# Kernel optimization log

Hardware: AMD Instinct MI355X
Metric: run time of the kernel (lower is better)

The kernel has to match this reference:

```python
import jax, jax.numpy as jnp
import numpy as np
from jax import lax

B, C, T, H, W = 1, 64, 16, 48, 48
RC = C // 16

def conv2d(x, w, b=None, stride=1, pad=1):
    out = lax.conv_general_dilated(x, w, (stride, stride), [(pad, pad), (pad, pad)],
                                   dimension_numbers=('NCHW', 'OIHW', 'NCHW'))
    return out if b is None else out + b[None, :, None, None]

def dwconv3d(x, w, b, pad, dil):
    out = lax.conv_general_dilated(x, w, (1, 1, 1), [(p, p) for p in pad], rhs_dilation=dil,
                                   dimension_numbers=('NCDHW', 'OIDHW', 'NCDHW'),
                                   feature_group_count=x.shape[1])
    return out + b[None, :, None, None, None]

def grid_sample_zeros(img, grid):
    # img [N,Cc,Hh,Ww], grid [N,Hg,Wg,2] with (x,y) in [-1,1]; bilinear, zeros padding, align_corners=False
    N, Cc, Hh, Ww = img.shape
    gx, gy = grid[..., 0], grid[..., 1]
    x = ((gx + 1.0) * Ww - 1.0) * 0.5
    y = ((gy + 1.0) * Hh - 1.0) * 0.5
    x0 = jnp.floor(x); y0 = jnp.floor(y)
    imgf = img.reshape(N, Cc, Hh * Ww)
    def corner(xi, yi, wgt):
        valid = (xi >= 0) & (xi < Ww) & (yi >= 0) & (yi < Hh)
        idx = (jnp.clip(yi, 0, Hh - 1) * Ww + jnp.clip(xi, 0, Ww - 1)).astype(jnp.int32)
        vals = jnp.take_along_axis(imgf, idx.reshape(N, 1, -1), axis=2).reshape(N, Cc, *xi.shape[1:])
        return vals * (wgt * valid)[:, None]
    return (corner(x0, y0, (x0 + 1 - x) * (y0 + 1 - y)) + corner(x0 + 1, y0, (x - x0) * (y0 + 1 - y))
            + corner(x0, y0 + 1, (x0 + 1 - x) * (y - y0)) + corner(x0 + 1, y0 + 1, (x - x0) * (y - y0)))

def corr_attn(a, w1, w2):
    avg = jnp.mean(a, axis=1, keepdims=True)
    mx = jnp.max(a, axis=1, keepdims=True)
    var = jnp.var(a, axis=1, keepdims=True, ddof=1)  # torch unbiased var
    y = jax.nn.sigmoid(conv2d(jnp.concatenate([avg, mx], axis=1), w1, pad=1) + conv2d(var, w2, pad=1))
    return a * y

def setup_inputs() -> dict:
    key = jax.random.key(0)
    ks = jax.random.split(key, 16)
    def n(k, shape, s=0.05):
        return jax.random.normal(k, shape, jnp.float32) * s
    return {
        'x': jax.random.normal(ks[0], (B, C, T, H, W), jnp.float32),
        'w_dc2': n(ks[1], (C, C)),
        'w_ofs_l': n(ks[2], (2, C, 3, 3)), 'b_ofs_l': n(ks[3], (2,)),
        'w_ofs_r': n(ks[4], (2, C, 3, 3)), 'b_ofs_r': n(ks[5], (2,)),
        'ca_w1': n(ks[6], (1, 2, 3, 3)), 'ca_w2': n(ks[7], (1, 1, 3, 3)),
        'w_down': n(ks[8], (RC, C)),
        'sa1_w': n(ks[9], (RC, 1, 9, 3, 3)), 'sa1_b': n(ks[10], (RC,)),
        'sa2_w': n(ks[11], (RC, 1, 9, 3, 3)), 'sa2_b': n(ks[12], (RC,)),
        'sa3_w': n(ks[13], (RC, 1, 9, 3, 3)), 'sa3_b': n(ks[14], (RC,)),
        'weights': jnp.ones(3, jnp.float32) / 3,
        'weights2': jnp.ones(2, jnp.float32) / 2,
        'w_back': n(ks[15], (C, RC)),
    }

def reference(x, w_dc2, w_ofs_l, b_ofs_l, w_ofs_r, b_ofs_r, ca_w1, ca_w2, w_down,
              sa1_w, sa1_b, sa2_w, sa2_b, sa3_w, sa3_b, weights, weights2, w_back):
    Bq, Cq, Tq, Hq, Wq = x.shape
    x2 = jnp.einsum('oc,bcthw->bothw', w_dc2, x)  # 1x1x1 conv3d
    left_move = jnp.concatenate([x2[:, :, 1:], x2[:, :, -1:]], axis=2)
    right_move = jnp.concatenate([x2[:, :, :1], x2[:, :, :-1]], axis=2)
    to2d = lambda t: t.transpose(0, 2, 1, 3, 4).reshape(Bq * Tq, Cq, Hq, Wq)
    off_l = conv2d(to2d(x + left_move), w_ofs_l, b_ofs_l, stride=2, pad=1)  # [BT,2,H2,W2]
    off_r = conv2d(to2d(x + right_move), w_ofs_r, b_ofs_r, stride=2, pad=1)
    H2, W2 = off_l.shape[-2:]
    gx, gy = jnp.meshgrid(jnp.arange(W2, dtype=x.dtype), jnp.arange(H2, dtype=x.dtype), indexing='xy')
    base = jnp.stack([gx, gy]) * 2.0  # [2,H2,W2]; matches create_grid_like * 2
    def norm_grid(v):  # faithful to normalize_grid (ch0 scaled by H2-1, ch1 by W2-1)
        gh = 2.0 * v[:, 0] / max(H2 - 1, 1) - 1.0
        gw = 2.0 * v[:, 1] / max(W2 - 1, 1) - 1.0
        return jnp.stack([gh, gw], axis=-1)
    left_part = grid_sample_zeros(to2d(left_move), norm_grid(base[None] + off_l))
    right_part = grid_sample_zeros(to2d(right_move), norm_grid(base[None] + off_r))
    to5d = lambda t: t.reshape(Bq, Tq, Cq, H2, W2).transpose(0, 2, 1, 3, 4)  # [B,C,T,H2,W2]
    left_part = to5d(left_part); right_part = to5d(right_part)
    def branch(part, wscale):
        aff = jnp.einsum('bcthw,bctsd->bthwsd', x, part)  # all-pairs correlation volume
        a = aff.reshape(Bq * Tq, Hq, Wq, H2 * W2).transpose(0, 3, 1, 2)
        a = corr_attn(a, ca_w1, ca_w2)
        a = a.reshape(Bq, Tq, H2, W2, Hq, Wq).transpose(0, 1, 4, 5, 2, 3)  # [B,T,H,W,H2,W2]
        return jnp.einsum('bctsd,bthwsd->bcthw', part, jax.nn.sigmoid(a) - 0.5) * wscale
    features = branch(left_part, weights2[0]) + branch(right_part, weights2[1])
    xd = jnp.einsum('oc,bcthw->bothw', w_down, x)  # channel reduction
    agg = (dwconv3d(xd, sa1_w, sa1_b, (4, 1, 1), (1, 1, 1)) * weights[0]
           + dwconv3d(xd, sa2_w, sa2_b, (4, 2, 2), (1, 2, 2)) * weights[1]
           + dwconv3d(xd, sa3_w, sa3_b, (4, 3, 3), (1, 3, 3)) * weights[2])
    agg = jnp.einsum('oc,bcthw->bothw', w_back, agg)
    return features * (jax.nn.sigmoid(agg) - 0.5)
```

## Files before the change

kernel.cpp:

```cpp
#include <hip/hip_runtime.h>
#include <hip/hip_bf16.h>

#define T_    16
#define C_    64
#define H_    48
#define W_    48
#define HW_   2304
#define THW_  36864
#define CTHW_ 2359296
#define H2_   24
#define W2_   24
#define SD_   576
#define RC_   4
#define SDT_  72

typedef short short8 __attribute__((ext_vector_type(8)));
typedef short short4v __attribute__((ext_vector_type(4)));
typedef float f32x4 __attribute__((ext_vector_type(4)));

__device__ __forceinline__ float sigm(float v) { return 1.f / (1.f + __expf(-v)); }
__device__ __forceinline__ unsigned short f2bf(float v) {
    __hip_bfloat16 h = __float2bfloat16(v);
    union { __hip_bfloat16 h; unsigned short u; } cv; cv.h = h; return cv.u;
}
__device__ __forceinline__ float bf2f(unsigned short u) {
    return __uint_as_float((unsigned)u << 16);
}

__global__ __launch_bounds__(256) void k_pre(const float* __restrict__ x,
                                             const float* __restrict__ w,
                                             const float* __restrict__ w_down,
                                             float* __restrict__ x2T,
                                             unsigned short* __restrict__ xbh,
                                             unsigned short* __restrict__ xbl,
                                             float* __restrict__ xd) {
    int base = blockIdx.x * 64;
    __shared__ float wl[64 * 65];
    __shared__ float xt[4096];
    __shared__ float ld[64 * 65];
    __shared__ float wd[256];
    int tid = threadIdx.x;
    for (int i = tid; i < 4096; i += 256) wl[(i >> 6) * 65 + (i & 63)] = w[i];
    for (int i = tid; i < 4096; i += 256) {
        float v = x[(size_t)(i >> 6) * THW_ + base + (i & 63)];
        xt[i] = v;
        ld[(i >> 6) * 65 + (i & 63)] = v;
    }
    if (tid < 256) wd[tid] = w_down[tid];
    __syncthreads();
    {
        int o_grp = tid >> 4, u_grp = tid & 15;
        float acc[4][4] = {};
        const float4* xt4 = (const float4*)xt;
        for (int c = 0; c < 64; ++c) {
            float xa[4];
            *(float4*)xa = xt4[c * 16 + u_grp];
            #pragma unroll
            for (int i = 0; i < 4; ++i) {
                float wv = wl[(o_grp * 4 + i) * 65 + c];
                #pragma unroll
                for (int g = 0; g < 4; ++g) acc[i][g] += wv * xa[g];
            }
        }
        #pragma unroll
        for (int g = 0; g < 4; ++g) {
            float4 v = make_float4(acc[0][g], acc[1][g], acc[2][g], acc[3][g]);
            *(float4*)&x2T[(size_t)(base + u_grp * 4 + g) * 64 + o_grp * 4] = v;
        }
    }
    {
        int r = tid >> 6, u = tid & 63;
        float a = 0.f;
        #pragma unroll 8
        for (int c = 0; c < 64; ++c) a += wd[r * 64 + c] * xt[c * 64 + u];
        xd[(size_t)r * THW_ + base + u] = a;
    }
    for (int i = tid; i < 4096; i += 256) {
        int u = i >> 6, c = i & 63;
        float v = ld[c * 65 + u];
        unsigned short h = f2bf(v);
        xbh[(size_t)(base + u) * 64 + c] = h;
        xbl[(size_t)(base + u) * 64 + c] = f2bf(v - bf2f(h));
    }
}

__global__ __launch_bounds__(256) void k_off(const unsigned short* __restrict__ xbh,
                                             const unsigned short* __restrict__ xbl,
                                             const float* __restrict__ x2T,
                                             const float* __restrict__ w_l,
                                             const float* __restrict__ b_l,
                                             const float* __restrict__ w_r,
                                             const float* __restrict__ b_r,
                                             float* __restrict__ off) {
    __shared__ float wlds[2304];
    int tid = threadIdx.x;
    for (int i = tid; i < 2304; i += 256) wlds[i] = (i < 1152) ? w_l[i] : w_r[i - 1152];
    __syncthreads();
    int wg = blockIdx.x * 4 + (tid >> 6);
    int lane = tid & 63;
    int j = wg % 24, i = (wg / 24) % 24, t = (wg / 576) % 16, side = wg / 9216;
    int ts = (side == 0) ? min(t + 1, T_ - 1) : max(t - 1, 0);
    const float* wp = wlds + side * 1152;
    const unsigned short* xhb = xbh + ((size_t)t * HW_) * 64 + lane;
    const unsigned short* xlb = xbl + ((size_t)t * HW_) * 64 + lane;
    const float* x2l = x2T + (size_t)ts * HW_ * 64 + lane;
    float a0 = 0.f, a1 = 0.f;
    for (int ki = 0; ki < 3; ++ki) {
        int hh = 2 * i - 1 + ki;
        if (hh < 0 || hh >= H_) continue;
        for (int kj = 0; kj < 3; ++kj) {
            int ww = 2 * j - 1 + kj;
            if (ww < 0 || ww >= W_) continue;
            int pos = hh * W_ + ww;
            float s = bf2f(xhb[(size_t)pos * 64]) + bf2f(xlb[(size_t)pos * 64])
                    + x2l[(size_t)pos * 64];
            int tap = ki * 3 + kj;
            a0 += s * wp[lane * 9 + tap];
            a1 += s * wp[576 + lane * 9 + tap];
        }
    }
    #pragma unroll
    for (int m = 32; m >= 1; m >>= 1) {
        a0 += __shfl_xor(a0, m);
        a1 += __shfl_xor(a1, m);
    }
    if (lane == 0) {
        const float* bb = (side == 0) ? b_l : b_r;
        int ob = (side * 16 + t) * 1152 + i * 24 + j;
        off[ob] = a0 + bb[0];
        off[ob + 576] = a1 + bb[1];
    }
}

__global__ __launch_bounds__(256) void k_gs(const float* __restrict__ x2T,
                                            const float* __restrict__ off,
                                            unsigned short* __restrict__ pch,
                                            unsigned short* __restrict__ pcl) {
    int wg = blockIdx.x * 4 + (threadIdx.x >> 6);
    int lane = threadIdx.x & 63;
    int sd = wg % 576;
    int t = (wg / 576) % 16;
    int side = wg / 9216;
    int d = sd % W2_, s = sd / W2_;
    const float* offp = off + (side * 16 + t) * 1152;
    float v0 = 2.f * (float)d + offp[sd];
    float v1 = 2.f * (float)s + offp[576 + sd];
    float xf = 48.f * v0 / 23.f - 0.5f;
    float yf = 48.f * v1 / 23.f - 0.5f;
    float x0 = floorf(xf), y0 = floorf(yf);
    int ix0 = (int)x0, iy0 = (int)y0;
    float fx = xf - x0, fy = yf - y0;
    float w00 = (1.f - fx) * (1.f - fy), w10 = fx * (1.f - fy);
    float w01 = (1.f - fx) * fy,         w11 = fx * fy;
    bool vx0 = (ix0 >= 0 && ix0 < W_), vx1 = (ix0 + 1 >= 0 && ix0 + 1 < W_);
    bool vy0 = (iy0 >= 0 && iy0 < H_), vy1 = (iy0 + 1 >= 0 && iy0 + 1 < H_);
    int cx0 = min(max(ix0, 0), W_ - 1), cx1 = min(max(ix0 + 1, 0), W_ - 1);
    int cy0 = min(max(iy0, 0), H_ - 1), cy1 = min(max(iy0 + 1, 0), H_ - 1);
    float m00 = (vx0 && vy0) ? w00 : 0.f;
    float m10 = (vx1 && vy0) ? w10 : 0.f;
    float m01 = (vx0 && vy1) ? w01 : 0.f;
    float m11 = (vx1 && vy1) ? w11 : 0.f;
    int ts = (side == 0) ? min(t + 1, T_ - 1) : max(t - 1, 0);
    const float* img = x2T + (size_t)ts * HW_ * 64;
    float val = m00 * img[(size_t)(cy0 * W_ + cx0) * 64 + lane]
              + m10 * img[(size_t)(cy0 * W_ + cx1) * 64 + lane]
              + m01 * img[(size_t)(cy1 * W_ + cx0) * 64 + lane]
              + m11 * img[(size_t)(cy1 * W_ + cx1) * 64 + lane];
    size_t idx = ((size_t)(side * 16 + t) * 576 + sd) * 64 + lane;
    unsigned short h = f2bf(val);
    pch[idx] = h;
    pcl[idx] = f2bf(val - bf2f(h));
}

__global__ __launch_bounds__(256) void k_stats(const unsigned short* __restrict__ xbh,
                                               const unsigned short* __restrict__ xbl,
                                               const unsigned short* __restrict__ pch,
                                               const unsigned short* __restrict__ pcl,
                                               float* __restrict__ stats) {
    int bid = blockIdx.x;
    int side = bid & 1;
    int tb = bid >> 1;
    int t = tb / 36, hwt = tb % 36;
    int base = t * HW_ + hwt * 64;
    __shared__ __attribute__((aligned(16))) unsigned short pah[2][64 * SDT_];
    __shared__ __attribute__((aligned(16))) unsigned short pal[2][64 * SDT_];
    int tid = threadIdx.x;
    int lane = tid & 63, wv = tid >> 6;
    int quad = lane >> 4, l15 = lane & 15;
    int m0 = wv * 16;
    const unsigned short* xrh = xbh + (size_t)(base + m0 + l15) * 64;
    const unsigned short* xrl = xbl + (size_t)(base + m0 + l15) * 64;
    short8 ah0 = *(const short8*)&xrh[quad * 8];
    short8 ah1 = *(const short8*)&xrh[32 + quad * 8];
    short8 al0 = *(const short8*)&xrl[quad * 8];
    short8 al1 = *(const short8*)&xrl[32 + quad * 8];
    int sH[4], sC[4];
    #pragma unroll
    for (int k = 0; k < 4; ++k) { int i = tid + k * 256; sH[k] = i >> 4; sC[k] = i & 15; }
    const unsigned short* phb = pch + (size_t)(side * 16 + t) * 576 * 64;
    const unsigned short* plb = pcl + (size_t)(side * 16 + t) * 576 * 64;
    uint2 pf_h[4], pf_l[4];
    #pragma unroll
    for (int k = 0; k < 4; ++k) {
        pf_h[k] = *(const uint2*)&phb[(size_t)sH[k] * 64 + sC[k] * 4];
        pf_l[k] = *(const uint2*)&plb[(size_t)sH[k] * 64 + sC[k] * 4];
    }
    float sum[4] = {}, sq[4] = {};
    float mx[4] = {-1e30f, -1e30f, -1e30f, -1e30f};
    for (int kt = 0; kt < 9; ++kt) {
        int b = kt & 1;
        #pragma unroll
        for (int k = 0; k < 4; ++k) {
            *(uint2*)&pah[b][sH[k] * SDT_ + sC[k] * 4] = pf_h[k];
            *(uint2*)&pal[b][sH[k] * SDT_ + sC[k] * 4] = pf_l[k];
        }
        if (kt < 8) {
            const unsigned short* ph = phb + (size_t)(kt + 1) * 64 * 64;
            const unsigned short* pl = plb + (size_t)(kt + 1) * 64 * 64;
            #pragma unroll
            for (int k = 0; k < 4; ++k) {
                pf_h[k] = *(const uint2*)&ph[(size_t)sH[k] * 64 + sC[k] * 4];
                pf_l[k] = *(const uint2*)&pl[(size_t)sH[k] * 64 + sC[k] * 4];
            }
        }
        __syncthreads();
        #pragma unroll
        for (int tile = 0; tile < 4; ++tile) {
            short8 bh0 = *(const short8*)&pah[b][(tile * 16 + l15) * SDT_ + quad * 8];
            short8 bh1 = *(const short8*)&pah[b][(tile * 16 + l15) * SDT_ + 32 + quad * 8];
            short8 bl0 = *(const short8*)&pal[b][(tile * 16 + l15) * SDT_ + quad * 8];
            short8 bl1 = *(const short8*)&pal[b][(tile * 16 + l15) * SDT_ + 32 + quad * 8];
            f32x4 dacc = {0.f, 0.f, 0.f, 0.f};
            dacc = __builtin_amdgcn_mfma_f32_16x16x32_bf16(ah0, bh0, dacc, 0, 0, 0);
            dacc = __builtin_amdgcn_mfma_f32_16x16x32_bf16(ah1, bh1, dacc, 0, 0, 0);
            dacc = __builtin_amdgcn_mfma_f32_16x16x32_bf16(ah0, bl0, dacc, 0, 0, 0);
            dacc = __builtin_amdgcn_mfma_f32_16x16x32_bf16(ah1, bl1, dacc, 0, 0, 0);
            dacc = __builtin_amdgcn_mfma_f32_16x16x32_bf16(al0, bh0, dacc, 0, 0, 0);
            dacc = __builtin_amdgcn_mfma_f32_16x16x32_bf16(al1, bh1, dacc, 0, 0, 0);
            #pragma unroll
            for (int r = 0; r < 4; ++r) {
                float v = dacc[r];
                sum[r] += v; sq[r] += v * v; mx[r] = fmaxf(mx[r], v);
            }
        }
    }
    #pragma unroll
    for (int m = 1; m < 16; m <<= 1)
        #pragma unroll
        for (int r = 0; r < 4; ++r) {
            sum[r] += __shfl_xor(sum[r], m);
            sq[r]  += __shfl_xor(sq[r], m);
            mx[r]   = fmaxf(mx[r], __shfl_xor(mx[r], m));
        }
    if (l15 == 0) {
        #pragma unroll
        for (int r = 0; r < 4; ++r) {
            int thw = base + m0 + quad * 4 + r;
            stats[(side * 3 + 0) * THW_ + thw] = sum[r] * (1.f / 576.f);
            stats[(side * 3 + 1) * THW_ + thw] = mx[r];
            stats[(side * 3 + 2) * THW_ + thw] =
                (sq[r] - sum[r] * sum[r] * (1.f / 576.f)) * (1.f / 575.f);
        }
    }
}

__global__ __launch_bounds__(256) void k_aux(const float* __restrict__ stats,
                      const float* __restrict__ ca_w1,
                      const float* __restrict__ ca_w2, float* __restrict__ yb,
                      const float* __restrict__ xd,
                      const float* __restrict__ w1, const float* __restrict__ b1,
                      const float* __restrict__ w2, const float* __restrict__ b2,
                      const float* __restrict__ w3, const float* __restrict__ b3,
                      const float* __restrict__ wts, float* __restrict__ agg0,
                      const unsigned short* __restrict__ pch,
                      unsigned short* __restrict__ partb) {
    __shared__ unsigned short ld[64 * 68];
    int blk = blockIdx.x;
    int tid = threadIdx.x;
    if (blk < (2 * THW_) / 256) {
        int idx = blk * 256 + tid;
        int side = idx / THW_, thw = idx % THW_;
        int w = thw % W_, h = (thw / W_) % H_, t = thw / HW_;
        const float* avg = stats + (side * 3 + 0) * THW_ + t * HW_;
        const float* mxp = stats + (side * 3 + 1) * THW_ + t * HW_;
        const float* var = stats + (side * 3 + 2) * THW_ + t * HW_;
        float acc = 0.f;
        for (int ki = 0; ki < 3; ++ki) {
            int hh = h - 1 + ki;
            if (hh < 0 || hh >= H_) continue;
            for (int kj = 0; kj < 3; ++kj) {
                int ww = w - 1 + kj;
                if (ww < 0 || ww >= W_) continue;
                int p = hh * W_ + ww;
                int kk = ki * 3 + kj;
                acc += ca_w1[kk] * avg[p] + ca_w1[9 + kk] * mxp[p] + ca_w2[kk] * var[p];
            }
        }
        yb[idx] = sigm(acc);
    } else if (blk < (2 * THW_) / 256 + (RC_ * THW_) / 256) {
        int idx = (blk - (2 * THW_) / 256) * 256 + tid;
        int w = idx % W_;
        int h = (idx / W_) % H_;
        int t = (idx / HW_) % T_;
        int r = idx / THW_;
        const float* xr = xd + r * THW_;
        const float* wk_arr[3] = {w1, w2, w3};
        const float* bs_arr[3] = {b1, b2, b3};
        float tot = 0.f;
        for (int m = 0; m < 3; ++m) {
            int dil = m + 1;
            float acc = bs_arr[m][r];
            const float* wk = wk_arr[m] + r * 81;
            for (int kt = 0; kt < 9; ++kt) {
                int tt = t - 4 + kt;
                if (tt < 0 || tt >= T_) continue;
                for (int kh = 0; kh < 3; ++kh) {
                    int hh = h + (kh - 1) * dil;
                    if (hh < 0 || hh >= H_) continue;
                    for (int kw = 0; kw < 3; ++kw) {
                        int wwp = w + (kw - 1) * dil;
                        if (wwp < 0 || wwp >= W_) continue;
                        acc += xr[tt * HW_ + hh * W_ + wwp] * wk[kt * 9 + kh * 3 + kw];
                    }
                }
            }
            tot += acc * wts[m];
        }
        agg0[idx] = tot;
    } else {
        int b2 = blk - ((2 * THW_) / 256 + (RC_ * THW_) / 256);
        int st = b2 / 9;
        int sdt = b2 % 9;
        const unsigned short* src = pch + ((size_t)st * 576 + sdt * 64) * 64;
        for (int i = tid; i < 4096; i += 256) ld[(i >> 6) * 68 + (i & 63)] = src[i];
        __syncthreads();
        unsigned short* dst = partb + (size_t)st * 64 * 576 + sdt * 64;
        for (int i = tid; i < 4096; i += 256) {
            int c = i >> 6, sdl = i & 63;
            dst[(size_t)c * 576 + sdl] = ld[sdl * 68 + c];
        }
    }
}

__global__ __launch_bounds__(256) void k_final(const unsigned short* __restrict__ xbh,
                                               const unsigned short* __restrict__ xbl,
                                               const unsigned short* __restrict__ pch,
                                               const unsigned short* __restrict__ pcl,
                                               const unsigned short* __restrict__ partb,
                                               const float* __restrict__ yb,
                                               const float* __restrict__ weights2,
                                               const float* __restrict__ agg0,
                                               const float* __restrict__ w_back,
                                               float* __restrict__ out) {
    int bid = blockIdx.x;
    int side = bid & 1;
    int tb = bid >> 1;
    int t = tb / 36, hwt = tb % 36;
    int base = t * HW_ + hwt * 64;
    int st = side * 16 + t;
    __shared__ __attribute__((aligned(16))) unsigned short pah[2][64 * SDT_];
    __shared__ __attribute__((aligned(16))) unsigned short pal[2][64 * SDT_];
    __shared__ __attribute__((aligned(16))) unsigned short wt[64 * SDT_];
    int tid = threadIdx.x;
    int lane = tid & 63, wv = tid >> 6;
    int quad = lane >> 4, l15 = lane & 15;
    int m0 = wv * 16;
    const unsigned short* xrh = xbh + (size_t)(base + m0 + l15) * 64;
    const unsigned short* xrl = xbl + (size_t)(base + m0 + l15) * 64;
    short8 ah0 = *(const short8*)&xrh[quad * 8];
    short8 ah1 = *(const short8*)&xrh[32 + quad * 8];
    short8 al0 = *(const short8*)&xrl[quad * 8];
    short8 al1 = *(const short8*)&xrl[32 + quad * 8];
    float yvs = yb[(size_t)side * THW_ + base + m0 + l15];
    int sH[4], sC[4];
    #pragma unroll
    for (int k = 0; k < 4; ++k) { int i = tid + k * 256; sH[k] = i >> 4; sC[k] = i & 15; }
    const unsigned short* phb = pch + (size_t)st * 576 * 64;
    const unsigned short* plb = pcl + (size_t)st * 576 * 64;
    const unsigned short* pbb = partb + (size_t)st * 64 * 576 + (size_t)(m0 + l15) * 576;
    uint2 pf_h[4], pf_l[4];
    short8 pbn0, pbn1;
    {
        #pragma unroll
        for (int k = 0; k < 4; ++k) {
            pf_h[k] = *(const uint2*)&phb[(size_t)sH[k] * 64 + sC[k] * 4];
            pf_l[k] = *(const uint2*)&plb[(size_t)sH[k] * 64 + sC[k] * 4];
        }
        pbn0 = *(const short8*)&pbb[quad * 8];
        pbn1 = *(const short8*)&pbb[32 + quad * 8];
    }
    f32x4 acc[4] = {};
    for (int kt = 0; kt < 9; ++kt) {
        int b = kt & 1;
        #pragma unroll
        for (int k = 0; k < 4; ++k) {
            *(uint2*)&pah[b][sH[k] * SDT_ + sC[k] * 4] = pf_h[k];
            *(uint2*)&pal[b][sH[k] * SDT_ + sC[k] * 4] = pf_l[k];
        }
        short8 pA0 = pbn0, pA1 = pbn1;
        if (kt < 8) {
            const unsigned short* ph = phb + (size_t)(kt + 1) * 64 * 64;
            const unsigned short* pl = plb + (size_t)(kt + 1) * 64 * 64;
            #pragma unroll
            for (int k = 0; k < 4; ++k) {
                pf_h[k] = *(const uint2*)&ph[(size_t)sH[k] * 64 + sC[k] * 4];
                pf_l[k] = *(const uint2*)&pl[(size_t)sH[k] * 64 + sC[k] * 4];
            }
            const unsigned short* pbr = pbb + (kt + 1) * 64;
            pbn0 = *(const short8*)&pbr[quad * 8];
            pbn1 = *(const short8*)&pbr[32 + quad * 8];
        }
        __syncthreads();
        #pragma unroll
        for (int tile = 0; tile < 4; ++tile) {
            short8 bh0 = *(const short8*)&pah[b][(tile * 16 + l15) * SDT_ + quad * 8];
            short8 bh1 = *(const short8*)&pah[b][(tile * 16 + l15) * SDT_ + 32 + quad * 8];
            short8 bl0 = *(const short8*)&pal[b][(tile * 16 + l15) * SDT_ + quad * 8];
            short8 bl1 = *(const short8*)&pal[b][(tile * 16 + l15) * SDT_ + 32 + quad * 8];
            f32x4 dacc = {0.f, 0.f, 0.f, 0.f};
            dacc = __builtin_amdgcn_mfma_f32_16x16x32_bf16(bh0, ah0, dacc, 0, 0, 0);
            dacc = __builtin_amdgcn_mfma_f32_16x16x32_bf16(bh1, ah1, dacc, 0, 0, 0);
            dacc = __builtin_amdgcn_mfma_f32_16x16x32_bf16(bl0, ah0, dacc, 0, 0, 0);
            dacc = __builtin_amdgcn_mfma_f32_16x16x32_bf16(bl1, ah1, dacc, 0, 0, 0);
            dacc = __builtin_amdgcn_mfma_f32_16x16x32_bf16(bh0, al0, dacc, 0, 0, 0);
            dacc = __builtin_amdgcn_mfma_f32_16x16x32_bf16(bh1, al1, dacc, 0, 0, 0);
            short4v wq;
            #pragma unroll
            for (int r = 0; r < 4; ++r)
                wq[r] = (short)f2bf(sigm(dacc[r] * yvs) - 0.5f);
            *(short4v*)&wt[(m0 + l15) * SDT_ + tile * 16 + quad * 4] = wq;
        }
        __syncthreads();
        #pragma unroll
        for (int tile = 0; tile < 4; ++tile) {
            short8 wb0 = *(const short8*)&wt[(tile * 16 + l15) * SDT_ + quad * 8];
            short8 wb1 = *(const short8*)&wt[(tile * 16 + l15) * SDT_ + 32 + quad * 8];
            acc[tile] = __builtin_amdgcn_mfma_f32_16x16x32_bf16(pA0, wb0, acc[tile], 0, 0, 0);
            acc[tile] = __builtin_amdgcn_mfma_f32_16x16x32_bf16(pA1, wb1, acc[tile], 0, 0, 0);
        }
    }
    float w2s = weights2[side];
    #pragma unroll
    for (int tile = 0; tile < 4; ++tile) {
        int thw = base + tile * 16 + l15;
        #pragma unroll
        for (int r = 0; r < 4; ++r) {
            int c = m0 + quad * 4 + r;
            float a = 0.f;
            #pragma unroll
            for (int rr = 0; rr < RC_; ++rr) a += w_back[c * RC_ + rr] * agg0[rr * THW_ + thw];
            atomicAdd(&out[(size_t)c * THW_ + thw],
                      acc[tile][r] * w2s * (sigm(a) - 0.5f));
        }
    }
}

extern "C" void kernel_launch(void* const* d_in, const int* in_sizes, int n_in,
                              void* d_out, int out_size, void* d_ws, size_t ws_size,
                              hipStream_t stream) {
    const float* x       = (const float*)d_in[0];
    const float* w_dc2   = (const float*)d_in[1];
    const float* w_ofs_l = (const float*)d_in[2];
    const float* b_ofs_l = (const float*)d_in[3];
    const float* w_ofs_r = (const float*)d_in[4];
    const float* b_ofs_r = (const float*)d_in[5];
    const float* ca_w1   = (const float*)d_in[6];
    const float* ca_w2   = (const float*)d_in[7];
    const float* w_down  = (const float*)d_in[8];
    const float* sa1_w   = (const float*)d_in[9];
    const float* sa1_b   = (const float*)d_in[10];
    const float* sa2_w   = (const float*)d_in[11];
    const float* sa2_b   = (const float*)d_in[12];
    const float* sa3_w   = (const float*)d_in[13];
    const float* sa3_b   = (const float*)d_in[14];
    const float* weights = (const float*)d_in[15];
    const float* weights2= (const float*)d_in[16];
    const float* w_back  = (const float*)d_in[17];
    float* out = (float*)d_out;

    float* ws    = (float*)d_ws;
    float* x2T   = ws;
    float* stats = x2T;
    float* yb    = stats + 2 * 3 * THW_;
    float* agg0  = yb + 2 * THW_;
    unsigned short* partb = (unsigned short*)(agg0 + RC_ * THW_);
    float* off   = ws + CTHW_;
    unsigned short* xbh = (unsigned short*)(off + 2 * T_ * 2 * SD_);
    unsigned short* xbl = xbh + CTHW_;
    unsigned short* pch = xbl + CTHW_;
    unsigned short* pcl = pch + 2 * 16 * 576 * 64;
    float* xd    = (float*)(pcl + 2 * 16 * 576 * 64);

    k_pre<<<THW_ / 64, 256, 0, stream>>>(x, w_dc2, w_down, x2T, xbh, xbl, xd);
    k_off<<<(2 * 16 * 576) / 4, 256, 0, stream>>>(xbh, xbl, x2T, w_ofs_l, b_ofs_l,
                                                  w_ofs_r, b_ofs_r, off);
    k_gs<<<(2 * 16 * 576) / 4, 256, 0, stream>>>(x2T, off, pch, pcl);
    k_stats<<<2 * 16 * 36, 256, 0, stream>>>(xbh, xbl, pch, pcl, stats);
    k_aux<<<(2 * THW_) / 256 + (RC_ * THW_) / 256 + 32 * 9, 256, 0, stream>>>(
        stats, ca_w1, ca_w2, yb, xd, sa1_w, sa1_b, sa2_w, sa2_b,
        sa3_w, sa3_b, weights, agg0, pch, partb);
    k_final<<<2 * 16 * 36, 256, 0, stream>>>(xbh, xbl, pch, pcl, partb, yb, weights2,
                                             agg0, w_back, out);
}
```

Before: 240.0 us.

## Load part operands directly from global, drop LDS staging, remap blocks for XCD locality

In k_stats and k_final, the double-buffered shared-memory staging of the part tiles (pch/pcl) is removed, and each wave now reads its B fragments straight from global memory, relying on L2 caching. The barriers and LDS traffic tied to staging go away, which lowers LDS use and may raise occupancy. Block indices are also remapped so consecutive hardware blocks spread across the 8 XCDs while blocks sharing a (side,t) slab land on the same one, which should improve cache reuse. The cost is redundant global loads across the four waves, and latency is no longer hidden by prefetch because the loop is not unrolled.

```diff
diff --git a/kernel.cpp b/kernel.cpp
--- a/kernel.cpp
+++ b/kernel.cpp
@@ -177,13 +177,11 @@
                                                const unsigned short* __restrict__ pch,
                                                const unsigned short* __restrict__ pcl,
                                                float* __restrict__ stats) {
-    int bid = blockIdx.x;
+    int bid = ((blockIdx.x & 7) * 144) + (blockIdx.x >> 3);
     int side = bid & 1;
     int tb = bid >> 1;
     int t = tb / 36, hwt = tb % 36;
     int base = t * HW_ + hwt * 64;
-    __shared__ __attribute__((aligned(16))) unsigned short pah[2][64 * SDT_];
-    __shared__ __attribute__((aligned(16))) unsigned short pal[2][64 * SDT_];
     int tid = threadIdx.x;
     int lane = tid & 63, wv = tid >> 6;
     int quad = lane >> 4, l15 = lane & 15;
@@ -194,42 +192,22 @@
     short8 ah1 = *(const short8*)&xrh[32 + quad * 8];
     short8 al0 = *(const short8*)&xrl[quad * 8];
     short8 al1 = *(const short8*)&xrl[32 + quad * 8];
-    int sH[4], sC[4];
-    #pragma unroll
-    for (int k = 0; k < 4; ++k) { int i = tid + k * 256; sH[k] = i >> 4; sC[k] = i & 15; }
     const unsigned short* phb = pch + (size_t)(side * 16 + t) * 576 * 64;
     const unsigned short* plb = pcl + (size_t)(side * 16 + t) * 576 * 64;
-    uint2 pf_h[4], pf_l[4];
-    #pragma unroll
-    for (int k = 0; k < 4; ++k) {
-        pf_h[k] = *(const uint2*)&phb[(size_t)sH[k] * 64 + sC[k] * 4];
-        pf_l[k] = *(const uint2*)&plb[(size_t)sH[k] * 64 + sC[k] * 4];
-    }
+    int foff = l15 * 64 + quad * 8;
     float sum[4] = {}, sq[4] = {};
     float mx[4] = {-1e30f, -1e30f, -1e30f, -1e30f};
+    #pragma unroll 1
     for (int kt = 0; kt < 9; ++kt) {
-        int b = kt & 1;
-        #pragma unroll
-        for (int k = 0; k < 4; ++k) {
-            *(uint2*)&pah[b][sH[k] * SDT_ + sC[k] * 4] = pf_h[k];
-            *(uint2*)&pal[b][sH[k] * SDT_ + sC[k] * 4] = pf_l[k];
-        }
-        if (kt < 8) {
-            const unsigned short* ph = phb + (size_t)(kt + 1) * 64 * 64;
-            const unsigned short* pl = plb + (size_t)(kt + 1) * 64 * 64;
-            #pragma unroll
-            for (int k = 0; k < 4; ++k) {
-                pf_h[k] = *(const uint2*)&ph[(size_t)sH[k] * 64 + sC[k] * 4];
-                pf_l[k] = *(const uint2*)&pl[(size_t)sH[k] * 64 + sC[k] * 4];
-            }
-        }
-        __syncthreads();
+        const unsigned short* ph = phb + (size_t)kt * 4096;
+        const unsigned short* pl = plb + (size_t)kt * 4096;
         #pragma unroll
         for (int tile = 0; tile < 4; ++tile) {
-            short8 bh0 = *(const short8*)&pah[b][(tile * 16 + l15) * SDT_ + quad * 8];
-            short8 bh1 = *(const short8*)&pah[b][(tile * 16 + l15) * SDT_ + 32 + quad * 8];
-            short8 bl0 = *(const short8*)&pal[b][(tile * 16 + l15) * SDT_ + quad * 8];
-            short8 bl1 = *(const short8*)&pal[b][(tile * 16 + l15) * SDT_ + 32 + quad * 8];
+            int fo = tile * 1024 + foff;
+            short8 bh0 = *(const short8*)&ph[fo];
+            short8 bh1 = *(const short8*)&ph[fo + 32];
+            short8 bl0 = *(const short8*)&pl[fo];
+            short8 bl1 = *(const short8*)&pl[fo + 32];
             f32x4 dacc = {0.f, 0.f, 0.f, 0.f};
             dacc = __builtin_amdgcn_mfma_f32_16x16x32_bf16(ah0, bh0, dacc, 0, 0, 0);
             dacc = __builtin_amdgcn_mfma_f32_16x16x32_bf16(ah1, bh1, dacc, 0, 0, 0);
@@ -352,14 +330,12 @@
                                                const float* __restrict__ agg0,
                                                const float* __restrict__ w_back,
                                                float* __restrict__ out) {
-    int bid = blockIdx.x;
+    int bid = ((blockIdx.x & 7) * 144) + (blockIdx.x >> 3);
     int side = bid & 1;
     int tb = bid >> 1;
     int t = tb / 36, hwt = tb % 36;
     int base = t * HW_ + hwt * 64;
     int st = side * 16 + t;
-    __shared__ __attribute__((aligned(16))) unsigned short pah[2][64 * SDT_];
-    __shared__ __attribute__((aligned(16))) unsigned short pal[2][64 * SDT_];
     __shared__ __attribute__((aligned(16))) unsigned short wt[64 * SDT_];
     int tid = threadIdx.x;
     int lane = tid & 63, wv = tid >> 6;
@@ -372,51 +348,25 @@
     short8 al0 = *(const short8*)&xrl[quad * 8];
     short8 al1 = *(const short8*)&xrl[32 + quad * 8];
     float yvs = yb[(size_t)side * THW_ + base + m0 + l15];
-    int sH[4], sC[4];
-    #pragma unroll
-    for (int k = 0; k < 4; ++k) { int i = tid + k * 256; sH[k] = i >> 4; sC[k] = i & 15; }
     const unsigned short* phb = pch + (size_t)st * 576 * 64;
     const unsigned short* plb = pcl + (size_t)st * 576 * 64;
     const unsigned short* pbb = partb + (size_t)st * 64 * 576 + (size_t)(m0 + l15) * 576;
-    uint2 pf_h[4], pf_l[4];
-    short8 pbn0, pbn1;
-    {
-        #pragma unroll
-        for (int k = 0; k < 4; ++k) {
-            pf_h[k] = *(const uint2*)&phb[(size_t)sH[k] * 64 + sC[k] * 4];
-            pf_l[k] = *(const uint2*)&plb[(size_t)sH[k] * 64 + sC[k] * 4];
-        }
-        pbn0 = *(const short8*)&pbb[quad * 8];
-        pbn1 = *(const short8*)&pbb[32 + quad * 8];
-    }
+    int foff = l15 * 64 + quad * 8;
+    short8 pbn0 = *(const short8*)&pbb[quad * 8];
+    short8 pbn1 = *(const short8*)&pbb[32 + quad * 8];
     f32x4 acc[4] = {};
+    #pragma unroll 1
     for (int kt = 0; kt < 9; ++kt) {
-        int b = kt & 1;
-        #pragma unroll
-        for (int k = 0; k < 4; ++k) {
-            *(uint2*)&pah[b][sH[k] * SDT_ + sC[k] * 4] = pf_h[k];
-            *(uint2*)&pal[b][sH[k] * SDT_ + sC[k] * 4] = pf_l[k];
-        }
-        short8 pA0 = pbn0, pA1 = pbn1;
-        if (kt < 8) {
-            const unsigned short* ph = phb + (size_t)(kt + 1) * 64 * 64;
-            const unsigned short* pl = plb + (size_t)(kt + 1) * 64 * 64;
-            #pragma unroll
-            for (int k = 0; k < 4; ++k) {
-                pf_h[k] = *(const uint2*)&ph[(size_t)sH[k] * 64 + sC[k] * 4];
-                pf_l[k] = *(const uint2*)&pl[(size_t)sH[k] * 64 + sC[k] * 4];
-            }
-            const unsigned short* pbr = pbb + (kt + 1) * 64;
-            pbn0 = *(const short8*)&pbr[quad * 8];
-            pbn1 = *(const short8*)&pbr[32 + quad * 8];
-        }
-        __syncthreads();
+        if (kt) __syncthreads();
+        const unsigned short* ph = phb + (size_t)kt * 4096;
+        const unsigned short* pl = plb + (size_t)kt * 4096;
         #pragma unroll
         for (int tile = 0; tile < 4; ++tile) {
-            short8 bh0 = *(const short8*)&pah[b][(tile * 16 + l15) * SDT_ + quad * 8];
-            short8 bh1 = *(const short8*)&pah[b][(tile * 16 + l15) * SDT_ + 32 + quad * 8];
-            short8 bl0 = *(const short8*)&pal[b][(tile * 16 + l15) * SDT_ + quad * 8];
-            short8 bl1 = *(const short8*)&pal[b][(tile * 16 + l15) * SDT_ + 32 + quad * 8];
+            int fo = tile * 1024 + foff;
+            short8 bh0 = *(const short8*)&ph[fo];
+            short8 bh1 = *(const short8*)&ph[fo + 32];
+            short8 bl0 = *(const short8*)&pl[fo];
+            short8 bl1 = *(const short8*)&pl[fo + 32];
             f32x4 dacc = {0.f, 0.f, 0.f, 0.f};
             dacc = __builtin_amdgcn_mfma_f32_16x16x32_bf16(bh0, ah0, dacc, 0, 0, 0);
             dacc = __builtin_amdgcn_mfma_f32_16x16x32_bf16(bh1, ah1, dacc, 0, 0, 0);
@@ -431,6 +381,12 @@
             *(short4v*)&wt[(m0 + l15) * SDT_ + tile * 16 + quad * 4] = wq;
         }
         __syncthreads();
+        short8 pA0 = pbn0, pA1 = pbn1;
+        if (kt < 8) {
+            const unsigned short* pbr = pbb + (kt + 1) * 64;
+            pbn0 = *(const short8*)&pbr[quad * 8];
+            pbn1 = *(const short8*)&pbr[32 + quad * 8];
+        }
         #pragma unroll
         for (int tile = 0; tile < 4; ++tile) {
             short8 wb0 = *(const short8*)&wt[(tile * 16 + l15) * SDT_ + quad * 8];
```

Result: slower. 351.2 us (+46.3%).
